# Optimization experiments

Measured on AMD Instinct MI355X. Metric: run time of the kernel, lower is better.

Reference implementation:

```python
import jax, jax.numpy as jnp
import numpy as np

B, S, D, H = 16, 4800, 256, 8
Dh = D // H
ATTN_EPS = 1e-6   # LinearAttention eps
LN_EPS = 1e-5     # nn.LayerNorm default eps


def _layer_norm(x, g, b):
    m = jnp.mean(x, axis=-1, keepdims=True)
    v = jnp.mean((x - m) ** 2, axis=-1, keepdims=True)
    return (x - m) * jax.lax.rsqrt(v + LN_EPS) * g + b


def setup_inputs() -> dict:
    key = jax.random.key(0)
    ks = jax.random.split(key, 8)
    sc_d = 1.0 / np.sqrt(D)
    sc_2d = 1.0 / np.sqrt(2 * D)
    return {
        "x": jax.random.normal(ks[0], (B, S, D), jnp.float32),
        "source": jax.random.normal(ks[1], (B, S, D), jnp.float32),
        "x_mask": jnp.ones((B, S), bool),
        "source_mask": jnp.ones((B, S), bool),
        # torch nn.Linear weights are [out_features, in_features]
        "Wq": jax.random.normal(ks[2], (D, D), jnp.float32) * sc_d,
        "Wk": jax.random.normal(ks[3], (D, D), jnp.float32) * sc_d,
        "Wv": jax.random.normal(ks[4], (D, D), jnp.float32) * sc_d,
        "Wm": jax.random.normal(ks[5], (D, D), jnp.float32) * sc_d,
        "W1": jax.random.normal(ks[6], (2 * D, 2 * D), jnp.float32) * sc_2d,
        "W2": jax.random.normal(ks[7], (D, 2 * D), jnp.float32) * sc_2d,
        "g_attn": jnp.ones((D,), jnp.float32),
        "b_attn": jnp.zeros((D,), jnp.float32),
        "g_ffn": jnp.ones((D,), jnp.float32),
        "b_ffn": jnp.zeros((D,), jnp.float32),
    }


def reference(x, source, x_mask, source_mask, Wq, Wk, Wv, Wm, W1, W2,
              g_attn, b_attn, g_ffn, b_ffn):
    Bn, Sn, Dm = x.shape
    # QKV projections (bias-free), split into heads: [B, S, H, Dh]
    q = (x @ Wq.T).reshape(Bn, Sn, H, Dh)
    k = (source @ Wk.T).reshape(Bn, Sn, H, Dh)
    v = (source @ Wv.T).reshape(Bn, Sn, H, Dh)
    # elu feature map
    q = jax.nn.elu(q) + 1.0
    k = jax.nn.elu(k) + 1.0
    qm = x_mask[:, :, None, None].astype(q.dtype)
    km = source_mask[:, :, None, None].astype(k.dtype)
    q = q * qm
    k = k * km
    v = v * km
    v = v / Sn
    # linear attention: kv outer product [B, H, Dh, Dh]
    kv = jnp.einsum('nshd,nshv->nhdv', k, v)
    z = 1.0 / (jnp.einsum('nlhd,nhd->nlh', q, k.sum(axis=1)) + ATTN_EPS)
    msg = jnp.einsum('nlhd,nhdv,nlh->nlhv', q, kv, z) * Sn  # [B, S, H, Dh]
    # merge + norm
    msg = msg.reshape(Bn, Sn, Dm) @ Wm.T
    msg = _layer_norm(msg, g_attn, b_attn)
    # FFN on concat([x, message]) -> 2D -> relu -> D, then norm
    h = jnp.concatenate([x, msg], axis=-1)
    h = jax.nn.relu(h @ W1.T) @ W2.T
    h = _layer_norm(h, g_ffn, b_ffn)
    return x + h
```

## Files before the change

### kernel.cpp

```cpp
#include <hip/hip_runtime.h>
#include <math.h>

#define BB 16
#define SS 4800
#define DD 256
#define HH 8
#define M_ROWS (BB * SS)
#define ATTN_EPS 1e-6f
#define LN_EPS 1e-5f
#define NCHUNK 10

typedef __attribute__((ext_vector_type(8))) __bf16 bf16x8;
typedef __attribute__((ext_vector_type(4))) float floatx4;
typedef unsigned short ushort;
typedef unsigned int uint;

__device__ __forceinline__ ushort f2bf(float f) {
    uint u = __builtin_bit_cast(uint, f);
    return (ushort)((u + 0x7fffu + ((u >> 16) & 1u)) >> 16);
}
__device__ __forceinline__ float bf2f(ushort h) {
    return __builtin_bit_cast(float, (uint)h << 16);
}
__device__ __forceinline__ void gload16(const ushort* g, ushort* l) {
    __builtin_amdgcn_global_load_lds(
        (const __attribute__((address_space(1))) uint*)g,
        (__attribute__((address_space(3))) uint*)l, 16, 0, 0);
}

__global__ __launch_bounds__(256) void mgemm(
    const ushort* __restrict__ A, int lda,
    const ushort* __restrict__ W, int ldw,
    float* __restrict__ Cf, ushort* __restrict__ Ch, int ldc,
    int K, int epi)
{
    __shared__ ushort As[128 * 32];
    __shared__ ushort Bs[128 * 32];
    const int tid = threadIdx.x;
    const int lane = tid & 63, wave = tid >> 6;
    const int wm = (wave & 1) * 64, wn = (wave >> 1) * 64;
    const int bm = blockIdx.x * 128, bn = blockIdx.y * 128;

    floatx4 acc[4][4] = {};

    const int srow_base = 32 * wave;
    const int lrow = lane >> 2;
    const int koff = (lane & 3) * 8;

    for (int k0 = 0; k0 < K; k0 += 32) {
#pragma unroll
        for (int c = 0; c < 2; ++c) {
            int row = srow_base + 16 * c + lrow;
            gload16(A + (size_t)(bm + row) * lda + k0 + koff, &As[(srow_base + 16 * c) * 32]);
            gload16(W + (size_t)(bn + row) * ldw + k0 + koff, &Bs[(srow_base + 16 * c) * 32]);
        }
        __syncthreads();
        const int fr = lane & 15, fk = (lane >> 4) * 8;
        bf16x8 a[4], b[4];
#pragma unroll
        for (int i = 0; i < 4; ++i) a[i] = *(const bf16x8*)&As[(wm + i * 16 + fr) * 32 + fk];
#pragma unroll
        for (int j = 0; j < 4; ++j) b[j] = *(const bf16x8*)&Bs[(wn + j * 16 + fr) * 32 + fk];
#pragma unroll
        for (int i = 0; i < 4; ++i)
#pragma unroll
            for (int j = 0; j < 4; ++j)
                acc[i][j] = __builtin_amdgcn_mfma_f32_16x16x32_bf16(a[i], b[j], acc[i][j], 0, 0, 0);
        __syncthreads();
    }

    const int cr = (lane >> 4) * 4, cc = lane & 15;
#pragma unroll
    for (int i = 0; i < 4; ++i)
#pragma unroll
        for (int j = 0; j < 4; ++j) {
            int m = bm + wm + i * 16 + cr;
            int n = bn + wn + j * 16 + cc;
#pragma unroll
            for (int r = 0; r < 4; ++r) {
                float v = acc[i][j][r];
                if (epi == 1)      v = (v > 0.f) ? (v + 1.f) : __expf(v);
                else if (epi == 2) v = (v > 0.f) ? v : 0.f;
                else if (epi == 3) { if (n < 256) v = (v > 0.f) ? (v + 1.f) : __expf(v); }
                if (Ch) Ch[(size_t)(m + r) * ldc + n] = f2bf(v);
                else    Cf[(size_t)(m + r) * ldc + n] = v;
            }
        }
}

__global__ __launch_bounds__(256) void attn_kernel(
    const ushort* q,
    const float* __restrict__ KV,
    const float* __restrict__ KS,
    ushort* msg)
{
    __shared__ float kvs[8 * 1028];
    __shared__ float kss[32 * 8];
    const int tid = threadIdx.x;
    const int bm = blockIdx.x * 64;
    const int b = bm / SS;

    for (int i = tid; i < 8192; i += 256) {
        int h = i >> 10, de = i & 1023;
        kvs[h * 1028 + de] = KV[(size_t)b * 8192 + i];
    }
    if (tid < 256) {
        int h = tid >> 5, d = tid & 31;
        kss[d * 8 + h] = KS[b * 256 + h * 32 + d];
    }
    __syncthreads();

    const int h = tid & 7;
    const int r0 = tid >> 3;
    const size_t m0 = bm + r0, m1 = bm + r0 + 32;

    float acc0[32] = {};
    float acc1[32] = {};
    float z0 = 0.f, z1 = 0.f;

    const uint4* q0p = (const uint4*)(q + m0 * 256 + h * 32);
    const uint4* q1p = (const uint4*)(q + m1 * 256 + h * 32);
    const float* kvh = &kvs[h * 1028];
    const float* ksh = &kss[h];

#pragma unroll
    for (int db = 0; db < 4; ++db) {
        uint4 qw0 = q0p[db];
        uint4 qw1 = q1p[db];
        uint qu0[4] = {qw0.x, qw0.y, qw0.z, qw0.w};
        uint qu1[4] = {qw1.x, qw1.y, qw1.z, qw1.w};
#pragma unroll
        for (int dd = 0; dd < 8; ++dd) {
            int d = db * 8 + dd;
            float qd0 = bf2f((ushort)(qu0[dd >> 1] >> ((dd & 1) * 16)));
            float qd1 = bf2f((ushort)(qu1[dd >> 1] >> ((dd & 1) * 16)));
            z0 += qd0 * ksh[d * 8];
            z1 += qd1 * ksh[d * 8];
            const float* kvd = kvh + d * 32;
#pragma unroll
            for (int e4 = 0; e4 < 8; ++e4) {
                float4 kv = *(const float4*)(kvd + e4 * 4);
                acc0[e4 * 4 + 0] += qd0 * kv.x; acc1[e4 * 4 + 0] += qd1 * kv.x;
                acc0[e4 * 4 + 1] += qd0 * kv.y; acc1[e4 * 4 + 1] += qd1 * kv.y;
                acc0[e4 * 4 + 2] += qd0 * kv.z; acc1[e4 * 4 + 2] += qd1 * kv.z;
                acc0[e4 * 4 + 3] += qd0 * kv.w; acc1[e4 * 4 + 3] += qd1 * kv.w;
            }
        }
    }

    float zi0 = 1.f / (z0 + ATTN_EPS);
    float zi1 = 1.f / (z1 + ATTN_EPS);
    uint4* o0 = (uint4*)(msg + m0 * 256 + h * 32);
    uint4* o1 = (uint4*)(msg + m1 * 256 + h * 32);
#pragma unroll
    for (int c = 0; c < 4; ++c) {
        uint4 pk;
        pk.x = (uint)f2bf(acc0[c*8+0]*zi0) | ((uint)f2bf(acc0[c*8+1]*zi0) << 16);
        pk.y = (uint)f2bf(acc0[c*8+2]*zi0) | ((uint)f2bf(acc0[c*8+3]*zi0) << 16);
        pk.z = (uint)f2bf(acc0[c*8+4]*zi0) | ((uint)f2bf(acc0[c*8+5]*zi0) << 16);
        pk.w = (uint)f2bf(acc0[c*8+6]*zi0) | ((uint)f2bf(acc0[c*8+7]*zi0) << 16);
        o0[c] = pk;
        pk.x = (uint)f2bf(acc1[c*8+0]*zi1) | ((uint)f2bf(acc1[c*8+1]*zi1) << 16);
        pk.y = (uint)f2bf(acc1[c*8+2]*zi1) | ((uint)f2bf(acc1[c*8+3]*zi1) << 16);
        pk.z = (uint)f2bf(acc1[c*8+4]*zi1) | ((uint)f2bf(acc1[c*8+5]*zi1) << 16);
        pk.w = (uint)f2bf(acc1[c*8+6]*zi1) | ((uint)f2bf(acc1[c*8+7]*zi1) << 16);
        o1[c] = pk;
    }
}

__global__ __launch_bounds__(256) void kv_part_kernel(
    const ushort* __restrict__ kvin,
    float* __restrict__ kvp, float* __restrict__ ksp)
{
    __shared__ float ks[16][32];
    __shared__ float vs[16][32];
    const int bh = blockIdx.x;
    const int chunk = blockIdx.y;
    const int b = bh >> 3, h = bh & 7;
    const int tid = threadIdx.x;
    const int d = tid >> 3;
    const int e0 = (tid & 7) * 4;
    const int s_base = chunk * (SS / NCHUNK);
    float acc[4] = {0.f, 0.f, 0.f, 0.f};
    float ksacc = 0.f;
    const int sl = tid >> 4;
    const int dd = (tid & 15) * 2;

    for (int s0 = 0; s0 < SS / NCHUNK; s0 += 16) {
        size_t off = ((size_t)(b * SS + s_base + s0 + sl)) * 512 + h * 32 + dd;
        uint ku = *(const uint*)(kvin + off);
        uint vu = *(const uint*)(kvin + off + 256);
        ks[sl][dd] = bf2f((ushort)ku); ks[sl][dd + 1] = bf2f((ushort)(ku >> 16));
        vs[sl][dd] = bf2f((ushort)vu); vs[sl][dd + 1] = bf2f((ushort)(vu >> 16));
        __syncthreads();
#pragma unroll
        for (int s = 0; s < 16; ++s) {
            float kd = ks[s][d];
            ksacc += kd;
#pragma unroll
            for (int j = 0; j < 4; ++j) acc[j] += kd * vs[s][e0 + j];
        }
        __syncthreads();
    }
    size_t base = ((size_t)bh * NCHUNK + chunk) * 1024;
#pragma unroll
    for (int j = 0; j < 4; ++j) kvp[base + d * 32 + e0 + j] = acc[j];
    if ((tid & 7) == 0) ksp[((size_t)bh * NCHUNK + chunk) * 32 + d] = ksacc;
}

__global__ __launch_bounds__(256) void kv_reduce_kernel(
    const float* __restrict__ kvp, const float* __restrict__ ksp,
    float* __restrict__ kv, float* __restrict__ ksum)
{
    const int bh = blockIdx.x;
    const int tid = threadIdx.x;
    for (int idx = tid; idx < 1024; idx += 256) {
        float s = 0.f;
        for (int c = 0; c < NCHUNK; ++c)
            s += kvp[((size_t)bh * NCHUNK + c) * 1024 + idx];
        kv[(size_t)bh * 1024 + idx] = s;
    }
    if (tid < 32) {
        float s = 0.f;
        for (int c = 0; c < NCHUNK; ++c)
            s += ksp[((size_t)bh * NCHUNK + c) * 32 + tid];
        ksum[bh * 32 + tid] = s;
    }
}

__global__ __launch_bounds__(256) void ln_kernel(
    const ushort* __restrict__ inh,
    const float* __restrict__ res,
    const ushort* __restrict__ resh, int rld, int roff,
    const float* __restrict__ g, const float* __restrict__ bt,
    float* __restrict__ outf, ushort* __restrict__ outh, int old, int ooff,
    int nrows)
{
    const int lane = threadIdx.x & 63;
    const int nwaves = (gridDim.x * blockDim.x) >> 6;
    const float4 gv = ((const float4*)g)[lane];
    const float4 bv = ((const float4*)bt)[lane];
    for (int row = (blockIdx.x * blockDim.x + threadIdx.x) >> 6; row < nrows;
         row += nwaves) {
        uint2 u = *(const uint2*)(inh + (size_t)row * 256 + lane * 4);
        float vx = bf2f((ushort)u.x), vy = bf2f((ushort)(u.x >> 16));
        float vz = bf2f((ushort)u.y), vw = bf2f((ushort)(u.y >> 16));
        float s = (vx + vy) + (vz + vw);
#pragma unroll
        for (int o = 1; o < 64; o <<= 1) s += __shfl_xor(s, o);
        float mean = s * (1.f / 256);
        float dx = vx - mean, dy = vy - mean, dz = vz - mean, dw = vw - mean;
        float q = (dx * dx + dy * dy) + (dz * dz + dw * dw);
#pragma unroll
        for (int o = 1; o < 64; o <<= 1) q += __shfl_xor(q, o);
        float rs = rsqrtf(q * (1.f / 256) + LN_EPS);
        float rx = dx * rs * gv.x + bv.x;
        float ry = dy * rs * gv.y + bv.y;
        float rz = dz * rs * gv.z + bv.z;
        float rw = dw * rs * gv.w + bv.w;
        if (res) {
            float4 rr = ((const float4*)(res + (size_t)row * 256))[lane];
            rx += rr.x; ry += rr.y; rz += rr.z; rw += rr.w;
        } else if (resh) {
            uint2 rr = *(const uint2*)(resh + (size_t)row * rld + roff + lane * 4);
            rx += bf2f((ushort)rr.x); ry += bf2f((ushort)(rr.x >> 16));
            rz += bf2f((ushort)rr.y); rw += bf2f((ushort)(rr.y >> 16));
        }
        if (outh) {
            uint2 pk;
            pk.x = (uint)f2bf(rx) | ((uint)f2bf(ry) << 16);
            pk.y = (uint)f2bf(rz) | ((uint)f2bf(rw) << 16);
            *(uint2*)(outh + (size_t)row * old + ooff + lane * 4) = pk;
        } else {
            float4 o4 = {rx, ry, rz, rw};
            *(float4*)(outf + (size_t)row * old + ooff + lane * 4) = o4;
        }
    }
}

__global__ __launch_bounds__(256) void cvt_flat(const float* __restrict__ src,
                                                ushort* __restrict__ dst, int n4)
{
    int i = blockIdx.x * 256 + threadIdx.x;
    if (i >= n4) return;
    float4 f = ((const float4*)src)[i];
    uint2 pk;
    pk.x = (uint)f2bf(f.x) | ((uint)f2bf(f.y) << 16);
    pk.y = (uint)f2bf(f.z) | ((uint)f2bf(f.w) << 16);
    ((uint2*)dst)[i] = pk;
}

__global__ __launch_bounds__(256) void cvt_x(const float* __restrict__ src,
                                             ushort* __restrict__ dst)
{
    int i = blockIdx.x * 256 + threadIdx.x;
    int row = i >> 6, c4 = i & 63;
    float4 f = ((const float4*)src)[i];
    uint2 pk;
    pk.x = (uint)f2bf(f.x) | ((uint)f2bf(f.y) << 16);
    pk.y = (uint)f2bf(f.z) | ((uint)f2bf(f.w) << 16);
    *(uint2*)(dst + (size_t)row * 512 + c4 * 4) = pk;
}

extern "C" void kernel_launch(void* const* d_in, const int* in_sizes, int n_in,
                              void* d_out, int out_size, void* d_ws, size_t ws_size,
                              hipStream_t stream)
{
    const float* x      = (const float*)d_in[0];
    const float* source = (const float*)d_in[1];
    const float* Wq = (const float*)d_in[4];
    const float* Wk = (const float*)d_in[5];
    const float* Wv = (const float*)d_in[6];
    const float* Wm = (const float*)d_in[7];
    const float* W1 = (const float*)d_in[8];
    const float* W2 = (const float*)d_in[9];
    const float* g_attn = (const float*)d_in[10];
    const float* b_attn = (const float*)d_in[11];
    const float* g_ffn  = (const float*)d_in[12];
    const float* b_ffn  = (const float*)d_in[13];
    float* out = (float*)d_out;

    char* p = (char*)d_ws;
    ushort* WB  = (ushort*)p;                 p += (size_t)655360 * 2;
    ushort* XC  = (ushort*)p;                 p += (size_t)M_ROWS * 512 * 2;
    ushort* SK  = (ushort*)p;                 p += (size_t)M_ROWS * 256 * 2;
    ushort* KVA = (ushort*)p;                 p += (size_t)M_ROWS * 512 * 2;
    ushort* Tb  = (ushort*)p;                 p += (size_t)M_ROWS * 256 * 2;
    float*  PKV = (float*)p;                  p += (size_t)BB * HH * NCHUNK * 1024 * 4;
    float*  PKS = (float*)p;                  p += (size_t)BB * HH * NCHUNK * 32 * 4;
    float*  KV  = (float*)p;                  p += (size_t)BB * HH * 1024 * 4;
    float*  KS  = (float*)p;                  p += (size_t)BB * HH * 32 * 4;
    ushort* Wqb = WB;
    ushort* Wkb = WB + 65536;
    ushort* Wvb = WB + 131072;
    ushort* Wmb = WB + 196608;
    ushort* W1b = WB + 262144;
    ushort* W2b = WB + 524288;
    ushort* KVb = KVA;
    ushort* Mrg = KVA;
    ushort* Hid = KVA;

    dim3 blk(256);

    cvt_x   <<<M_ROWS * 64 / 256, blk, 0, stream>>>(x, XC);
    cvt_flat<<<M_ROWS * 64 / 256, blk, 0, stream>>>(source, SK, M_ROWS * 64);
    cvt_flat<<<64,  blk, 0, stream>>>(Wq, Wqb, 16384);
    cvt_flat<<<64,  blk, 0, stream>>>(Wk, Wkb, 16384);
    cvt_flat<<<64,  blk, 0, stream>>>(Wv, Wvb, 16384);
    cvt_flat<<<64,  blk, 0, stream>>>(Wm, Wmb, 16384);
    cvt_flat<<<256, blk, 0, stream>>>(W1, W1b, 65536);
    cvt_flat<<<128, blk, 0, stream>>>(W2, W2b, 32768);

    mgemm<<<dim3(600, 4), blk, 0, stream>>>(SK, 256, Wkb, 256, nullptr, KVb, 512, 256, 3);

    kv_part_kernel<<<dim3(BB * HH, NCHUNK), blk, 0, stream>>>(KVb, PKV, PKS);
    kv_reduce_kernel<<<BB * HH, blk, 0, stream>>>(PKV, PKS, KV, KS);

    mgemm<<<dim3(600, 2), blk, 0, stream>>>(XC, 512, Wqb, 256, nullptr, SK, 256, 256, 1);

    attn_kernel<<<M_ROWS / 64, blk, 0, stream>>>(SK, KV, KS, SK);

    mgemm<<<dim3(600, 2), blk, 0, stream>>>(SK, 256, Wmb, 256, nullptr, Mrg, 256, 256, 0);
    ln_kernel<<<2048, blk, 0, stream>>>(Mrg, nullptr, nullptr, 0, 0, g_attn, b_attn,
                                        nullptr, XC, 512, 256, M_ROWS);

    mgemm<<<dim3(600, 4), blk, 0, stream>>>(XC, 512, W1b, 512, nullptr, Hid, 512, 512, 2);
    mgemm<<<dim3(600, 2), blk, 0, stream>>>(Hid, 512, W2b, 512, nullptr, Tb, 256, 512, 0);

    ln_kernel<<<2048, blk, 0, stream>>>(Tb, nullptr, XC, 512, 0, g_ffn, b_ffn,
                                        out, nullptr, 256, 0, M_ROWS);
}
```

Before: 617.2 us.

## Fuse layer norm into Wm and W2 GEMM epilogues with full-row tiles

Adds a GEMM kernel whose block covers a full 256-column row tile, so each block can compute row mean and variance from its accumulators through shuffles and shared memory. LayerNorm plus the residual add then run in the epilogue. This removes the two standalone LN kernels and the bf16 intermediate round trips for Mrg and Tb. The catch is a one-pass E[x^2]-mean^2 variance, a grid of only 600 blocks with 32 accumulators per thread (more register pressure), and scalar, less coalesced epilogue stores. The final residual now comes from the fp32 x rather than the bf16 copy.

```diff
diff --git a/kernel.cpp b/kernel.cpp
--- a/kernel.cpp
+++ b/kernel.cpp
@@ -84,6 +84,110 @@
                 else if (epi == 3) { if (n < 256) v = (v > 0.f) ? (v + 1.f) : __expf(v); }
                 if (Ch) Ch[(size_t)(m + r) * ldc + n] = f2bf(v);
                 else    Cf[(size_t)(m + r) * ldc + n] = v;
+            }
+        }
+}
+
+__global__ __launch_bounds__(256) void mgemm_ln(
+    const ushort* __restrict__ A, int lda,
+    const ushort* __restrict__ W,
+    int K,
+    const float* __restrict__ res,
+    const float* __restrict__ g, const float* __restrict__ bt,
+    float* __restrict__ outf, ushort* __restrict__ outh, int old, int ooff)
+{
+    __shared__ ushort As[128 * 32];
+    __shared__ ushort Bs[256 * 32];
+    const int tid = threadIdx.x;
+    const int lane = tid & 63, wave = tid >> 6;
+    const int wm = (wave & 1) * 64, wn = (wave >> 1) * 128;
+    const int bm = blockIdx.x * 128;
+
+    floatx4 acc[4][8] = {};
+
+    const int lrow = lane >> 2;
+    const int koff = (lane & 3) * 8;
+
+    for (int k0 = 0; k0 < K; k0 += 32) {
+#pragma unroll
+        for (int c = 0; c < 2; ++c) {
+            int row = 32 * wave + 16 * c + lrow;
+            gload16(A + (size_t)(bm + row) * lda + k0 + koff,
+                    &As[(32 * wave + 16 * c) * 32]);
+        }
+#pragma unroll
+        for (int c = 0; c < 4; ++c) {
+            int row = 64 * wave + 16 * c + lrow;
+            gload16(W + (size_t)row * K + k0 + koff,
+                    &Bs[(64 * wave + 16 * c) * 32]);
+        }
+        __syncthreads();
+        const int fr = lane & 15, fk = (lane >> 4) * 8;
+        bf16x8 a[4], b[8];
+#pragma unroll
+        for (int i = 0; i < 4; ++i) a[i] = *(const bf16x8*)&As[(wm + i * 16 + fr) * 32 + fk];
+#pragma unroll
+        for (int j = 0; j < 8; ++j) b[j] = *(const bf16x8*)&Bs[(wn + j * 16 + fr) * 32 + fk];
+#pragma unroll
+        for (int i = 0; i < 4; ++i)
+#pragma unroll
+            for (int j = 0; j < 8; ++j)
+                acc[i][j] = __builtin_amdgcn_mfma_f32_16x16x32_bf16(a[i], b[j], acc[i][j], 0, 0, 0);
+        __syncthreads();
+    }
+
+    const int cr = (lane >> 4) * 4, cc = lane & 15;
+    float* redS = (float*)As;
+    float* redQ = redS + 256;
+
+#pragma unroll
+    for (int i = 0; i < 4; ++i)
+#pragma unroll
+        for (int r = 0; r < 4; ++r) {
+            float s = 0.f, q = 0.f;
+#pragma unroll
+            for (int j = 0; j < 8; ++j) {
+                float v = acc[i][j][r];
+                s += v; q += v * v;
+            }
+#pragma unroll
+            for (int o = 1; o < 16; o <<= 1) {
+                s += __shfl_xor(s, o);
+                q += __shfl_xor(q, o);
+            }
+            if (cc == 0) {
+                int row = wm + i * 16 + cr + r;
+                redS[(wave >> 1) * 128 + row] = s;
+                redQ[(wave >> 1) * 128 + row] = q;
+            }
+        }
+    __syncthreads();
+
+    float gj[8], bj[8];
+#pragma unroll
+    for (int j = 0; j < 8; ++j) {
+        gj[j] = g[wn + j * 16 + cc];
+        bj[j] = bt[wn + j * 16 + cc];
+    }
+
+#pragma unroll
+    for (int i = 0; i < 4; ++i)
+#pragma unroll
+        for (int r = 0; r < 4; ++r) {
+            int row = wm + i * 16 + cr + r;
+            float s = redS[row] + redS[128 + row];
+            float q = redQ[row] + redQ[128 + row];
+            float mean = s * (1.f / 256);
+            float var = q * (1.f / 256) - mean * mean;
+            float rs = rsqrtf(var + LN_EPS);
+            size_t m = bm + row;
+#pragma unroll
+            for (int j = 0; j < 8; ++j) {
+                int n = wn + j * 16 + cc;
+                float v = (acc[i][j][r] - mean) * rs * gj[j] + bj[j];
+                if (res) v += res[m * 256 + n];
+                if (outh) outh[m * old + ooff + n] = f2bf(v);
+                else      outf[m * old + ooff + n] = v;
             }
         }
 }
@@ -228,56 +332,6 @@
     }
 }
 
-__global__ __launch_bounds__(256) void ln_kernel(
-    const ushort* __restrict__ inh,
-    const float* __restrict__ res,
-    const ushort* __restrict__ resh, int rld, int roff,
-    const float* __restrict__ g, const float* __restrict__ bt,
-    float* __restrict__ outf, ushort* __restrict__ outh, int old, int ooff,
-    int nrows)
-{
-    const int lane = threadIdx.x & 63;
-    const int nwaves = (gridDim.x * blockDim.x) >> 6;
-    const float4 gv = ((const float4*)g)[lane];
-    const float4 bv = ((const float4*)bt)[lane];
-    for (int row = (blockIdx.x * blockDim.x + threadIdx.x) >> 6; row < nrows;
-         row += nwaves) {
-        uint2 u = *(const uint2*)(inh + (size_t)row * 256 + lane * 4);
-        float vx = bf2f((ushort)u.x), vy = bf2f((ushort)(u.x >> 16));
-        float vz = bf2f((ushort)u.y), vw = bf2f((ushort)(u.y >> 16));
-        float s = (vx + vy) + (vz + vw);
-#pragma unroll
-        for (int o = 1; o < 64; o <<= 1) s += __shfl_xor(s, o);
-        float mean = s * (1.f / 256);
-        float dx = vx - mean, dy = vy - mean, dz = vz - mean, dw = vw - mean;
-        float q = (dx * dx + dy * dy) + (dz * dz + dw * dw);
-#pragma unroll
-        for (int o = 1; o < 64; o <<= 1) q += __shfl_xor(q, o);
-        float rs = rsqrtf(q * (1.f / 256) + LN_EPS);
-        float rx = dx * rs * gv.x + bv.x;
-        float ry = dy * rs * gv.y + bv.y;
-        float rz = dz * rs * gv.z + bv.z;
-        float rw = dw * rs * gv.w + bv.w;
-        if (res) {
-            float4 rr = ((const float4*)(res + (size_t)row * 256))[lane];
-            rx += rr.x; ry += rr.y; rz += rr.z; rw += rr.w;
-        } else if (resh) {
-            uint2 rr = *(const uint2*)(resh + (size_t)row * rld + roff + lane * 4);
-            rx += bf2f((ushort)rr.x); ry += bf2f((ushort)(rr.x >> 16));
-            rz += bf2f((ushort)rr.y); rw += bf2f((ushort)(rr.y >> 16));
-        }
-        if (outh) {
-            uint2 pk;
-            pk.x = (uint)f2bf(rx) | ((uint)f2bf(ry) << 16);
-            pk.y = (uint)f2bf(rz) | ((uint)f2bf(rw) << 16);
-            *(uint2*)(outh + (size_t)row * old + ooff + lane * 4) = pk;
-        } else {
-            float4 o4 = {rx, ry, rz, rw};
-            *(float4*)(outf + (size_t)row * old + ooff + lane * 4) = o4;
-        }
-    }
-}
-
 __global__ __launch_bounds__(256) void cvt_flat(const float* __restrict__ src,
                                                 ushort* __restrict__ dst, int n4)
 {
@@ -325,7 +379,6 @@
     ushort* XC  = (ushort*)p;                 p += (size_t)M_ROWS * 512 * 2;
     ushort* SK  = (ushort*)p;                 p += (size_t)M_ROWS * 256 * 2;
     ushort* KVA = (ushort*)p;                 p += (size_t)M_ROWS * 512 * 2;
-    ushort* Tb  = (ushort*)p;                 p += (size_t)M_ROWS * 256 * 2;
     float*  PKV = (float*)p;                  p += (size_t)BB * HH * NCHUNK * 1024 * 4;
     float*  PKS = (float*)p;                  p += (size_t)BB * HH * NCHUNK * 32 * 4;
     float*  KV  = (float*)p;                  p += (size_t)BB * HH * 1024 * 4;
@@ -337,7 +390,6 @@
     ushort* W1b = WB + 262144;
     ushort* W2b = WB + 524288;
     ushort* KVb = KVA;
-    ushort* Mrg = KVA;
     ushort* Hid = KVA;
 
     dim3 blk(256);
@@ -360,13 +412,11 @@
 
     attn_kernel<<<M_ROWS / 64, blk, 0, stream>>>(SK, KV, KS, SK);
 
-    mgemm<<<dim3(600, 2), blk, 0, stream>>>(SK, 256, Wmb, 256, nullptr, Mrg, 256, 256, 0);
-    ln_kernel<<<2048, blk, 0, stream>>>(Mrg, nullptr, nullptr, 0, 0, g_attn, b_attn,
-                                        nullptr, XC, 512, 256, M_ROWS);
+    mgemm_ln<<<600, blk, 0, stream>>>(SK, 256, Wmb, 256, nullptr,
+                                      g_attn, b_attn, nullptr, XC, 512, 256);
 
     mgemm<<<dim3(600, 4), blk, 0, stream>>>(XC, 512, W1b, 512, nullptr, Hid, 512, 512, 2);
-    mgemm<<<dim3(600, 2), blk, 0, stream>>>(Hid, 512, W2b, 512, nullptr, Tb, 256, 512, 0);
-
-    ln_kernel<<<2048, blk, 0, stream>>>(Tb, nullptr, XC, 512, 0, g_ffn, b_ffn,
-                                        out, nullptr, 256, 0, M_ROWS);
-}
+
+    mgemm_ln<<<600, blk, 0, stream>>>(Hid, 512, W2b, 512, x,
+                                      g_ffn, b_ffn, out, nullptr, 256, 0);
+}
```

New measurement: 774.7 us. 25.5% more time.
